# Kernel tuning notes

Measured on AMD Instinct MI355X. Metric: run time of the kernel, lower is better.

The kernel has to match this reference:

```python
import jax, jax.numpy as jnp
import numpy as np

EPS = 1e-8
LOSS_EPS = 1e-6
LOSS_WEIGHT = 1.0
N_BOXES = 262144

# ---------- rotated-2D-box helpers (mmcv diff_iou_rotated style) ----------

def box2corners_2d(box):
    # box: (N,5) = (x, y, w, h, alpha) -> corners (N,4,2), CCW order
    x, y, w, h, a = box[:, 0], box[:, 1], box[:, 2], box[:, 3], box[:, 4]
    x4 = jnp.array([0.5, -0.5, -0.5, 0.5], box.dtype) * w[:, None]   # (N,4)
    y4 = jnp.array([0.5, 0.5, -0.5, -0.5], box.dtype) * h[:, None]
    c, s = jnp.cos(a)[:, None], jnp.sin(a)[:, None]
    rx = x4 * c - y4 * s + x[:, None]
    ry = x4 * s + y4 * c + y[:, None]
    return jnp.stack([rx, ry], axis=-1)


def box_intersection(c1, c2):
    # segment-segment intersections between the 4 edges of each box
    # c1, c2: (N,4,2) -> pts (N,16,2), mask (N,16)
    l1 = jnp.concatenate([c1, jnp.roll(c1, -1, axis=1)], axis=-1)[:, :, None, :]  # (N,4,1,4)
    l2 = jnp.concatenate([c2, jnp.roll(c2, -1, axis=1)], axis=-1)[:, None, :, :]  # (N,1,4,4)
    x1, y1, x2, y2 = l1[..., 0], l1[..., 1], l1[..., 2], l1[..., 3]
    x3, y3, x4, y4 = l2[..., 0], l2[..., 1], l2[..., 2], l2[..., 3]
    num = (y4 - y3) * (x2 - x1) - (x4 - x3) * (y2 - y1)
    den_t = (x4 - x3) * (y1 - y3) - (y4 - y3) * (x1 - x3)
    den_u = (x2 - x1) * (y1 - y3) - (y2 - y1) * (x1 - x3)
    safe = jnp.where(num == 0.0, 1.0, num)
    t = jnp.where(num == 0.0, -1.0, den_t / safe)
    u = jnp.where(num == 0.0, -1.0, -den_u / safe)
    mask = (t > 0.0) & (t < 1.0) & (u > 0.0) & (u < 1.0)  # (N,4,4)
    t2 = den_t / (num + EPS)
    pts = jnp.stack([x1 + t2 * (x2 - x1), y1 + t2 * (y2 - y1)], axis=-1)
    pts = pts * mask[..., None]
    n = c1.shape[0]
    return pts.reshape(n, 16, 2), mask.reshape(n, 16)


def box_in_box(c1, c2):
    # which corners of box1 lie inside box2; c1,c2: (N,4,2) -> (N,4) bool
    a, b, d = c2[:, 0:1], c2[:, 1:2], c2[:, 3:4]
    ab, ad, am = b - a, d - a, c1 - a
    p_ab = jnp.sum(ab * am, -1) / jnp.sum(ab * ab, -1)
    p_ad = jnp.sum(ad * am, -1) / jnp.sum(ad * ad, -1)
    tol = 1e-6
    return (p_ab > -tol) & (p_ab < 1 + tol) & (p_ad > -tol) & (p_ad < 1 + tol)


def polygon_area(vertices, mask):
    # sort valid vertices CCW around their mean, close polygon, shoelace area
    # vertices: (N,24,2), mask: (N,24) bool -> area (N,)
    maskf = mask.astype(vertices.dtype)
    nv = jnp.maximum(jnp.sum(maskf, axis=1, keepdims=True), 1.0)
    mean = jnp.sum(vertices * maskf[..., None], axis=1, keepdims=True) / nv[..., None]
    v = vertices - mean
    ang = jnp.arctan2(v[..., 1], v[..., 0])
    # invalid vertices get huge, index-increasing keys so they sort last (stable)
    ang = jnp.where(mask, ang, 1e6 + jnp.arange(24, dtype=vertices.dtype))
    order = jnp.argsort(ang, axis=1)                         # (N,24) int
    vs = jnp.take_along_axis(v, order[..., None], axis=1)    # (N,24,2)
    ms = jnp.take_along_axis(mask, order, axis=1)
    first = vs[:, 0:1]                                       # first (valid) vertex
    vs = jnp.where(ms[..., None], vs, first)                 # pad closes polygon
    x, y = vs[..., 0], vs[..., 1]
    xn, yn = jnp.roll(x, -1, axis=1), jnp.roll(y, -1, axis=1)
    return 0.5 * jnp.abs(jnp.sum(x * yn - y * xn, axis=1))


def diff_iou_rotated_3d(b1, b2):
    # b1, b2: (N,7) = (x,y,z,w,h,l,alpha) -> IoU3D (N,)
    c1 = box2corners_2d(b1[:, jnp.array([0, 1, 3, 4, 6])])
    c2 = box2corners_2d(b2[:, jnp.array([0, 1, 3, 4, 6])])
    ipts, imask = box_intersection(c1, c2)
    m12 = box_in_box(c1, c2)
    m21 = box_in_box(c2, c1)
    vertices = jnp.concatenate([c1, c2, ipts], axis=1)   # (N,24,2)
    mask = jnp.concatenate([m12, m21, imask], axis=1)    # (N,24)
    inter_2d = polygon_area(vertices, mask)
    zmax1, zmin1 = b1[:, 2] + 0.5 * b1[:, 5], b1[:, 2] - 0.5 * b1[:, 5]
    zmax2, zmin2 = b2[:, 2] + 0.5 * b2[:, 5], b2[:, 2] - 0.5 * b2[:, 5]
    z_ov = jnp.maximum(jnp.minimum(zmax1, zmax2) - jnp.maximum(zmin1, zmin2), 0.0)
    inter_3d = inter_2d * z_ov
    vol1 = b1[:, 3] * b1[:, 4] * b1[:, 5]
    vol2 = b2[:, 3] * b2[:, 4] * b2[:, 5]
    return inter_3d / (vol1 + vol2 - inter_3d)


def corners_from_bboxes3d(b):
    # (N,7) -> (N,8,3); rotation about axis=1 (mmdet3d rotation_3d_in_axis)
    corners_norm = jnp.array([[-0.5, -0.5, -0.5], [-0.5, -0.5, 0.5],
                              [-0.5, 0.5, 0.5], [-0.5, 0.5, -0.5],
                              [0.5, -0.5, -0.5], [0.5, -0.5, 0.5],
                              [0.5, 0.5, 0.5], [0.5, 0.5, -0.5]], b.dtype)
    corners = corners_norm[None] * b[:, None, 3:6]          # (N,8,3)
    c, s = jnp.cos(b[:, 6])[:, None], jnp.sin(b[:, 6])[:, None]
    x, y, z = corners[..., 0], corners[..., 1], corners[..., 2]
    xr = x * c + z * s
    zr = -x * s + z * c
    return jnp.stack([xr, y, zr], axis=-1) + b[:, None, :3]


def diou_3d_loss(pred, target):
    iou3d = jnp.nan_to_num(diff_iou_rotated_3d(pred, target), nan=0.0)
    ctd = jnp.sum((pred[:, :3] - target[:, :3]) ** 2, axis=-1)
    cnd = jnp.mean(jnp.sum((corners_from_bboxes3d(pred)
                            - corners_from_bboxes3d(target)) ** 2, axis=-1), axis=1)
    did = jnp.sum(target[:, 3:6] ** 2, axis=-1)
    return 1.0 - iou3d + (ctd + cnd) / (ctd + cnd + did + LOSS_EPS)


def setup_inputs() -> dict:
    key = jax.random.key(0)
    k1, k2, k3, k4, k5 = jax.random.split(key, 5)
    xy = jax.random.uniform(k1, (N_BOXES, 2), minval=-40.0, maxval=40.0)
    z = jax.random.uniform(k2, (N_BOXES, 1), minval=-3.0, maxval=1.0)
    dims = jax.random.uniform(k3, (N_BOXES, 3), minval=0.8, maxval=4.0)
    ang = jax.random.uniform(k4, (N_BOXES, 1), minval=-np.pi, maxval=np.pi)
    target = jnp.concatenate([xy, z, dims, ang], axis=1).astype(jnp.float32)
    noise = jax.random.normal(k5, (N_BOXES, 7), jnp.float32) * \
        jnp.array([0.3, 0.3, 0.1, 0.2, 0.2, 0.2, 0.1], jnp.float32)
    pred = target + noise
    pred = pred.at[:, 3:6].set(jnp.maximum(pred[:, 3:6], 0.1))
    return {"pred": pred, "target": target}


def reference(pred, target):
    # DIOU3DLoss.forward with weight=None, reduction='mean'
    return LOSS_WEIGHT * jnp.mean(diou_3d_loss(pred, target))
```

## Files before the change

### kernel.cpp

```cpp
#include <hip/hip_runtime.h>
#include <math.h>

#define EPSI 1e-8f
#define TOLI 1e-6f

typedef __fp16 half2v __attribute__((ext_vector_type(2)));

__device__ __forceinline__ float frcp(float x) { return __builtin_amdgcn_rcpf(x); }

#define CE(A, B) {                                  \
    unsigned ka = key[A], kb = key[B];              \
    key[A] = ka < kb ? ka : kb;                     \
    key[B] = ka < kb ? kb : ka; }

__global__ __launch_bounds__(256, 4) void diou3d_main(
    const float* __restrict__ pred, const float* __restrict__ tgt,
    float* __restrict__ partial, int n)
{
    __shared__ unsigned vbuf[24][256];
    __shared__ float wsum[4];
    int tx = threadIdx.x;
    int tid = blockIdx.x * 256 + tx;
    float loss = 0.0f;
    if (tid < n) {
        const float* P = pred + (size_t)tid * 7;
        const float* T = tgt  + (size_t)tid * 7;
        float p0 = P[0], p1 = P[1], p2 = P[2], p3 = P[3], p4 = P[4], p5 = P[5], p6 = P[6];
        float t0 = T[0], t1 = T[1], t2 = T[2], t3 = T[3], t4 = T[4], t5 = T[5], t6 = T[6];

        float sp, cp, st, ct;
        __sincosf(p6, &sp, &cp);
        __sincosf(t6, &st, &ct);
        const float hx[4] = {0.5f, -0.5f, -0.5f, 0.5f};
        const float hy[4] = {0.5f, 0.5f, -0.5f, -0.5f};
        float c1x[4], c1y[4], c2x[4], c2y[4];
#pragma unroll
        for (int k = 0; k < 4; k++) {
            float xa = hx[k] * p3, ya = hy[k] * p4;
            c1x[k] = xa * cp - ya * sp + p0;
            c1y[k] = xa * sp + ya * cp + p1;
            float xb = hx[k] * t3, yb = hy[k] * t4;
            c2x[k] = xb * ct - yb * st + t0;
            c2y[k] = xb * st + yb * ct + t1;
        }

        float vx[24], vy[24];
        float ma[24];

        {
            float abx = c2x[1] - c2x[0], aby = c2y[1] - c2y[0];
            float adx = c2x[3] - c2x[0], ady = c2y[3] - c2y[0];
            float rab = frcp(abx * abx + aby * aby);
            float rad = frcp(adx * adx + ady * ady);
#pragma unroll
            for (int k = 0; k < 4; k++) {
                float amx = c1x[k] - c2x[0], amy = c1y[k] - c2y[0];
                float pab = (abx * amx + aby * amy) * rab;
                float pad = (adx * amx + ady * amy) * rad;
                bool m = (pab > -TOLI) && (pab < 1.0f + TOLI) && (pad > -TOLI) && (pad < 1.0f + TOLI);
                ma[k] = m ? 1.0f : 0.0f;
                vx[k] = c1x[k]; vy[k] = c1y[k];
            }
        }
        {
            float abx = c1x[1] - c1x[0], aby = c1y[1] - c1y[0];
            float adx = c1x[3] - c1x[0], ady = c1y[3] - c1y[0];
            float rab = frcp(abx * abx + aby * aby);
            float rad = frcp(adx * adx + ady * ady);
#pragma unroll
            for (int k = 0; k < 4; k++) {
                float amx = c2x[k] - c1x[0], amy = c2y[k] - c1y[0];
                float pab = (abx * amx + aby * amy) * rab;
                float pad = (adx * amx + ady * amy) * rad;
                bool m = (pab > -TOLI) && (pab < 1.0f + TOLI) && (pad > -TOLI) && (pad < 1.0f + TOLI);
                ma[4 + k] = m ? 1.0f : 0.0f;
                vx[4 + k] = c2x[k]; vy[4 + k] = c2y[k];
            }
        }

#pragma unroll
        for (int i = 0; i < 4; i++) {
            float x1 = c1x[i], y1 = c1y[i];
            float dx12 = c1x[(i + 1) & 3] - x1, dy12 = c1y[(i + 1) & 3] - y1;
#pragma unroll
            for (int j = 0; j < 4; j++) {
                float x3 = c2x[j], y3 = c2y[j];
                float dx34 = c2x[(j + 1) & 3] - x3, dy34 = c2y[(j + 1) & 3] - y3;
                float num  = dy34 * dx12 - dx34 * dy12;
                float dxs = x1 - x3, dys = y1 - y3;
                float den_t = dx34 * dys - dy34 * dxs;
                float den_u = dx12 * dys - dy12 * dxs;
                bool m = (den_t * num > 0.0f) && ((num - den_t) * num > 0.0f)
                      && (den_u * num < 0.0f) && ((num + den_u) * num > 0.0f);
                float t2d = den_t * frcp(num + EPSI);
                int idx = 8 + i * 4 + j;
                vx[idx] = x1 + t2d * dx12;
                vy[idx] = y1 + t2d * dy12;
                ma[idx] = m ? 1.0f : 0.0f;
            }
        }

        float cntf = 0.0f, sx = 0.0f, sy = 0.0f;
#pragma unroll
        for (int k = 0; k < 24; k++) {
            cntf += ma[k];
            sx = fmaf(ma[k], vx[k], sx);
            sy = fmaf(ma[k], vy[k], sy);
        }
        int ic = (int)cntf;
        float rnv = frcp(fmaxf(cntf, 1.0f));
        float mx = sx * rnv, my = sy * rnv;

        unsigned key[24];
#pragma unroll
        for (int k = 0; k < 24; k++) {
            float ux = vx[k] - mx, uy = vy[k] - my;
            half2v h = __builtin_amdgcn_cvt_pkrtz(ux, uy);
            vbuf[k][tx] = __builtin_bit_cast(unsigned, h);
            float d = fabsf(ux) + fabsf(uy);
            float pq = ux * frcp(d);
            pq = (d == 0.0f) ? 0.0f : pq;
            float ang = (uy < 0.0f) ? (pq - 1.0f) : (1.0f - pq);
            unsigned u = __float_as_uint(ang);
            u ^= (unsigned)(((int)u >> 31)) | 0x80000000u;
            unsigned kk = (u & 0xFFFFFFE0u) | (unsigned)k;
            key[k] = (ma[k] != 0.0f) ? kk : (0xFFFFFFE0u | (unsigned)k);
        }

#pragma unroll
        for (int p = 1; p < 32; p <<= 1) {
#pragma unroll
            for (int k = p; k >= 1; k >>= 1) {
#pragma unroll
                for (int j = k & (p - 1); j + k < 32; j += 2 * k) {
#pragma unroll
                    for (int i = 0; i < k; i++) {
                        int lo = i + j, hi = i + j + k;
                        if (hi < 24 && (lo / (2 * p) == hi / (2 * p))) {
                            CE(lo, hi);
                        }
                    }
                }
            }
        }

        float gx[12], gy[12];
#pragma unroll
        for (int s = 0; s < 12; s++) {
            int idx = (int)(key[s] & 31u);
            half2v h = __builtin_bit_cast(half2v, vbuf[idx][tx]);
            gx[s] = (float)h.x; gy[s] = (float)h.y;
        }

        float x0 = gx[0], y0 = gy[0];
#pragma unroll
        for (int s = 0; s < 12; s++) {
            bool v = (s < ic);
            gx[s] = v ? gx[s] : x0;
            gy[s] = v ? gy[s] : y0;
        }
        float area2 = 0.0f;
#pragma unroll
        for (int s = 0; s < 12; s++) {
            int ns = (s == 11) ? 0 : s + 1;
            area2 += gx[s] * gy[ns] - gy[s] * gx[ns];
        }
        float inter2d = 0.5f * fabsf(area2);

        float zmax1 = p2 + 0.5f * p5, zmin1 = p2 - 0.5f * p5;
        float zmax2 = t2 + 0.5f * t5, zmin2 = t2 - 0.5f * t5;
        float zov = fmaxf(fminf(zmax1, zmax2) - fmaxf(zmin1, zmin2), 0.0f);
        float inter3d = inter2d * zov;
        float vol1 = p3 * p4 * p5, vol2 = t3 * t4 * t5;
        float iou = inter3d / (vol1 + vol2 - inter3d);
        if (isnan(iou)) iou = 0.0f;

        float d0 = p0 - t0, d1 = p1 - t1, d2 = p2 - t2;
        float ctd = d0 * d0 + d1 * d1 + d2 * d2;

        float cosd = cp * ct + sp * st;
        float dp2 = p3 * p3 + p4 * p4 + p5 * p5;
        float dt2 = t3 * t3 + t4 * t4 + t5 * t5;
        float crossd = p3 * t3 * cosd + p4 * t4 + p5 * t5 * cosd;
        float cnd = ctd + 0.25f * (dp2 + dt2) - 0.5f * crossd;

        float dterm = (ctd + cnd) / (ctd + cnd + dt2 + 1e-6f);
        loss = 1.0f - iou + dterm;
    }

#pragma unroll
    for (int off = 32; off > 0; off >>= 1) loss += __shfl_down(loss, off);
    int lane = tx & 63, wid = tx >> 6;
    if (lane == 0) wsum[wid] = loss;
    __syncthreads();
    if (tx == 0)
        partial[blockIdx.x] = wsum[0] + wsum[1] + wsum[2] + wsum[3];
}

__global__ __launch_bounds__(256) void diou3d_reduce(
    const float* __restrict__ partial, int nblocks, float* __restrict__ out, float invn)
{
    float s = 0.0f;
    for (int i = threadIdx.x; i < nblocks; i += 256) s += partial[i];
#pragma unroll
    for (int off = 32; off > 0; off >>= 1) s += __shfl_down(s, off);
    __shared__ float wsum[4];
    int lane = threadIdx.x & 63, wid = threadIdx.x >> 6;
    if (lane == 0) wsum[wid] = s;
    __syncthreads();
    if (threadIdx.x == 0)
        out[0] = (wsum[0] + wsum[1] + wsum[2] + wsum[3]) * invn;
}

extern "C" void kernel_launch(void* const* d_in, const int* in_sizes, int n_in,
                              void* d_out, int out_size, void* d_ws, size_t ws_size,
                              hipStream_t stream) {
    const float* pred = (const float*)d_in[0];
    const float* tgt  = (const float*)d_in[1];
    float* out = (float*)d_out;
    int n = in_sizes[0] / 7;
    const int T = 256;
    int blocks = (n + T - 1) / T;
    float* partial = (float*)d_ws;
    diou3d_main<<<blocks, T, 0, stream>>>(pred, tgt, partial, n);
    diou3d_reduce<<<1, 256, 0, stream>>>(partial, blocks, out, 1.0f / (float)n);
}
```

Baseline: 78.67 us.

## Share edge cross-products for segment intersections and derive box-in-box masks from them

```diff
diff --git a/kernel.cpp b/kernel.cpp
--- a/kernel.cpp
+++ b/kernel.cpp
@@ -2,7 +2,6 @@
 #include <math.h>
 
 #define EPSI 1e-8f
-#define TOLI 1e-6f
 
 typedef __fp16 half2v __attribute__((ext_vector_type(2)));
 
@@ -47,58 +46,77 @@
         float vx[24], vy[24];
         float ma[24];
 
-        {
-            float abx = c2x[1] - c2x[0], aby = c2y[1] - c2y[0];
-            float adx = c2x[3] - c2x[0], ady = c2y[3] - c2y[0];
-            float rab = frcp(abx * abx + aby * aby);
-            float rad = frcp(adx * adx + ady * ady);
-#pragma unroll
-            for (int k = 0; k < 4; k++) {
-                float amx = c1x[k] - c2x[0], amy = c1y[k] - c2y[0];
-                float pab = (abx * amx + aby * amy) * rab;
-                float pad = (adx * amx + ady * amy) * rad;
-                bool m = (pab > -TOLI) && (pab < 1.0f + TOLI) && (pad > -TOLI) && (pad < 1.0f + TOLI);
-                ma[k] = m ? 1.0f : 0.0f;
-                vx[k] = c1x[k]; vy[k] = c1y[k];
+#pragma unroll
+        for (int k = 0; k < 4; k++) {
+            vx[k] = c1x[k];     vy[k] = c1y[k];
+            vx[4 + k] = c2x[k]; vy[4 + k] = c2y[k];
+        }
+
+        float e1x[2], e1y[2], e2x[2], e2y[2];
+        e1x[0] = c1x[1] - c1x[0]; e1y[0] = c1y[1] - c1y[0];
+        e1x[1] = c1x[2] - c1x[1]; e1y[1] = c1y[2] - c1y[1];
+        e2x[0] = c2x[1] - c2x[0]; e2y[0] = c2y[1] - c2y[0];
+        e2x[1] = c2x[2] - c2x[1]; e2y[1] = c2y[2] - c2y[1];
+
+        float rb[2][2];
+#pragma unroll
+        for (int a = 0; a < 2; a++)
+#pragma unroll
+            for (int b = 0; b < 2; b++) {
+                float bn = e2y[b] * e1x[a] - e2x[b] * e1y[a];
+                rb[a][b] = frcp(bn + EPSI);
             }
-        }
-        {
-            float abx = c1x[1] - c1x[0], aby = c1y[1] - c1y[0];
-            float adx = c1x[3] - c1x[0], ady = c1y[3] - c1y[0];
-            float rab = frcp(abx * abx + aby * aby);
-            float rad = frcp(adx * adx + ady * ady);
-#pragma unroll
-            for (int k = 0; k < 4; k++) {
-                float amx = c2x[k] - c1x[0], amy = c2y[k] - c1y[0];
-                float pab = (abx * amx + aby * amy) * rab;
-                float pad = (adx * amx + ady * amy) * rad;
-                bool m = (pab > -TOLI) && (pab < 1.0f + TOLI) && (pad > -TOLI) && (pad < 1.0f + TOLI);
-                ma[4 + k] = m ? 1.0f : 0.0f;
-                vx[4 + k] = c2x[k]; vy[4 + k] = c2y[k];
+
+        float A_[2][4], Bv[4], C_[2][4], Dv[4];
+#pragma unroll
+        for (int b = 0; b < 2; b++)
+#pragma unroll
+            for (int i = 0; i < 4; i++)
+                A_[b][i] = e2x[b] * c1y[i] - e2y[b] * c1x[i];
+#pragma unroll
+        for (int j = 0; j < 4; j++)
+            Bv[j] = e2x[j & 1] * c2y[j] - e2y[j & 1] * c2x[j];
+#pragma unroll
+        for (int a = 0; a < 2; a++)
+#pragma unroll
+            for (int j = 0; j < 4; j++)
+                C_[a][j] = e1x[a] * c2y[j] - e1y[a] * c2x[j];
+#pragma unroll
+        for (int i = 0; i < 4; i++)
+            Dv[i] = e1x[i & 1] * c1y[i] - e1y[i & 1] * c1x[i];
+
+        float hmn[4], hmx[4];
+#pragma unroll
+        for (int i = 0; i < 4; i++) {
+            float gmn = 0.0f, gmx = 0.0f;
+#pragma unroll
+            for (int j = 0; j < 4; j++) {
+                const int a = i & 1, b = j & 1;
+                float g = A_[b][i] - Bv[j];
+                float h = C_[a][j] - Dv[i];
+                float r = rb[a][b];
+                float tau = g * r;
+                float ups = h * r;
+                bool mt = (i < 2) ? (tau > 0.0f && tau < 1.0f)
+                                  : (tau > -1.0f && tau < 0.0f);
+                bool mu = (j < 2) ? (ups > 0.0f && ups < 1.0f)
+                                  : (ups > -1.0f && ups < 0.0f);
+                const int idx = 8 + i * 4 + j;
+                vx[idx] = fmaf(tau, e1x[a], c1x[i]);
+                vy[idx] = fmaf(tau, e1y[a], c1y[i]);
+                ma[idx] = (mt && mu) ? 1.0f : 0.0f;
+                if (j == 0) gmn = g; else if (j == 1) gmn = fminf(gmn, g);
+                else if (j == 2) gmx = g; else gmx = fmaxf(gmx, g);
+                if (i == 0) hmn[j] = h;
+                else if (i == 1) hmn[j] = fminf(hmn[j], h);
+                else if (i == 2) hmx[j] = h;
+                else hmx[j] = fmaxf(hmx[j], h);
             }
-        }
-
-#pragma unroll
-        for (int i = 0; i < 4; i++) {
-            float x1 = c1x[i], y1 = c1y[i];
-            float dx12 = c1x[(i + 1) & 3] - x1, dy12 = c1y[(i + 1) & 3] - y1;
-#pragma unroll
-            for (int j = 0; j < 4; j++) {
-                float x3 = c2x[j], y3 = c2y[j];
-                float dx34 = c2x[(j + 1) & 3] - x3, dy34 = c2y[(j + 1) & 3] - y3;
-                float num  = dy34 * dx12 - dx34 * dy12;
-                float dxs = x1 - x3, dys = y1 - y3;
-                float den_t = dx34 * dys - dy34 * dxs;
-                float den_u = dx12 * dys - dy12 * dxs;
-                bool m = (den_t * num > 0.0f) && ((num - den_t) * num > 0.0f)
-                      && (den_u * num < 0.0f) && ((num + den_u) * num > 0.0f);
-                float t2d = den_t * frcp(num + EPSI);
-                int idx = 8 + i * 4 + j;
-                vx[idx] = x1 + t2d * dx12;
-                vy[idx] = y1 + t2d * dy12;
-                ma[idx] = m ? 1.0f : 0.0f;
-            }
-        }
+            ma[i] = (gmn >= 0.0f && gmx <= 0.0f) ? 1.0f : 0.0f;
+        }
+#pragma unroll
+        for (int j = 0; j < 4; j++)
+            ma[4 + j] = (hmn[j] >= 0.0f && hmx[j] <= 0.0f) ? 1.0f : 0.0f;
 
         float cntf = 0.0f, sx = 0.0f, sy = 0.0f;
 #pragma unroll
```

New measurement: 75.16 us. 4.5% less time.
